# Performance work log

Hardware: AMD Instinct MI355X
Metric: run time of the kernel (lower is better)

## Reference

```python
import jax, jax.numpy as jnp
import numpy as np

B, I, O, G = 4096, 256, 256, 32


def setup_inputs() -> dict:
    key = jax.random.key(0)
    k1, k2, k3, k4 = jax.random.split(key, 4)
    x = jax.random.normal(k1, (B, I), dtype=jnp.float32)
    fouriercoeffs = jax.random.normal(k2, (2, O, I, G), dtype=jnp.float32) / (np.sqrt(I) * np.sqrt(G))
    bias = jnp.zeros((1, O), dtype=jnp.float32)
    mask = jnp.ones((I, O), dtype=jnp.float32)
    # scale_base = mu/sqrt(I) + sigma*(rand*2-1)/sqrt(I), mu=0, sigma=1
    scale_base = (jax.random.uniform(k3, (I, O), dtype=jnp.float32) * 2.0 - 1.0) / np.sqrt(I)
    scale_fft = jnp.ones((I, O), dtype=jnp.float32) * (1.0 / np.sqrt(I)) * mask
    return {"x": x, "fouriercoeffs": fouriercoeffs, "bias": bias, "mask": mask,
            "scale_base": scale_base, "scale_fft": scale_fft}


def reference(x, fouriercoeffs, bias, mask, scale_base, scale_fft):
    gridsize = fouriercoeffs.shape[-1]
    k = jnp.arange(1, gridsize + 1, dtype=x.dtype)          # (G,)
    kx = x[:, :, None] * k                                   # (B, I, G)
    c = jnp.cos(kx)
    s = jnp.sin(kx)
    # einsum 'dbik,djik->bij' with d=2 split into cos/sin parts
    y = jnp.einsum('bik,jik->bij', c, fouriercoeffs[0]) \
        + jnp.einsum('bik,jik->bij', s, fouriercoeffs[1])    # (B, I, O)
    base = jax.nn.silu(x)                                     # SiLU base branch
    y = scale_base[None, :, :] * base[:, :, None] + scale_fft[None, :, :] * y
    y = (mask[None, :, :] * y).sum(axis=1)                    # sum over inputdim -> (B, O)
    y = y + bias
    return y
```

## Files before the change

### kernel.cpp

```cpp
#include <hip/hip_runtime.h>
#include <stdint.h>


#define I_DIM 256
#define O_DIM 256
#define G_DIM 32
#define B_DIM 4096

#define BM 128
#define BN 128
#define KSPLIT 16
#define ICH 16
#define PITCH 72

typedef short s8v __attribute__((ext_vector_type(8)));
typedef float f4v __attribute__((ext_vector_type(4)));

__device__ __forceinline__ uint32_t pack2bf16(float a, float b) {
  uint32_t ua = __builtin_bit_cast(uint32_t, a);
  uint32_t ub = __builtin_bit_cast(uint32_t, b);
  ua += 0x7FFFu + ((ua >> 16) & 1u);
  ub += 0x7FFFu + ((ub >> 16) & 1u);
  return (ua >> 16) | (ub & 0xFFFF0000u);
}
__device__ __forceinline__ unsigned short bf16_rne(float a) {
  uint32_t ua = __builtin_bit_cast(uint32_t, a);
  ua += 0x7FFFu + ((ua >> 16) & 1u);
  return (unsigned short)(ua >> 16);
}
__device__ __forceinline__ uint32_t cvtpk_bf16(float a, float b) {
  uint32_t r;
  asm("v_cvt_pk_bf16_f32 %0, %1, %2" : "=v"(r) : "v"(a), "v"(b));
  return r;
}
__device__ __forceinline__ float silu_f(float v) { return v / (1.0f + __expf(-v)); }

__device__ __forceinline__ void gen_feat_store(float xv, uint4* Ar, int c0, int xr) {
  const int half = c0 >> 2;
  float s1, c1, s17, c17;
  __sincosf(xv, &s1, &c1);
  __sincosf(17.f * xv, &s17, &c17);
  const float m2 = 2.f * c1;
  float fA0 = half ? s1 : c1;
  float fA1 = m2 * fA0 - (half ? 0.f : 1.f);
  float fB0 = half ? s17 : c17;
  float fB1 = half ? (s17 * c1 + c17 * s1)
                   : (c17 * c1 - s17 * s1);
  #pragma unroll
  for (int q = 0; q < 2; ++q) {
    uint32_t wa0 = cvtpk_bf16(fA0, fA1);
    uint32_t wb0 = cvtpk_bf16(fB0, fB1);
    float tA2 = m2 * fA1 - fA0, tB2 = m2 * fB1 - fB0;
    float tA3 = m2 * tA2 - fA1, tB3 = m2 * tB2 - fB1;
    uint32_t wa1 = cvtpk_bf16(tA2, tA3);
    uint32_t wb1 = cvtpk_bf16(tB2, tB3);
    fA0 = m2 * tA3 - tA2;  fB0 = m2 * tB3 - tB2;
    fA1 = m2 * fA0 - tA3;  fB1 = m2 * fB0 - tB3;
    uint32_t wa2 = cvtpk_bf16(fA0, fA1);
    uint32_t wb2 = cvtpk_bf16(fB0, fB1);
    float uA2 = m2 * fA1 - fA0, uB2 = m2 * fB1 - fB0;
    float uA3 = m2 * uA2 - fA1, uB3 = m2 * uB2 - fB1;
    uint32_t wa3 = cvtpk_bf16(uA2, uA3);
    uint32_t wb3 = cvtpk_bf16(uB2, uB3);
    Ar[(c0 + q) ^ xr]     = make_uint4(wa0, wa1, wa2, wa3);
    Ar[(c0 + 2 + q) ^ xr] = make_uint4(wb0, wb1, wb2, wb3);
    fA0 = m2 * uA3 - uA2;  fB0 = m2 * uB3 - uB2;
    fA1 = m2 * fA0 - uA3;  fB1 = m2 * fB0 - uB3;
  }
}

__global__ __launch_bounds__(256) void prep_bs_kernel(
    const float* __restrict__ fc, const float* __restrict__ mask,
    const float* __restrict__ sfft, short* __restrict__ Bp)
{
  const int gid = blockIdx.x * 256 + threadIdx.x;
  const int e = gid & 3;
  const int p = gid >> 2;
  const int i = p >> 8, j = p & 255;
  const int d = e >> 1;
  const int koff = (e & 1) * 16;
  const size_t ij = (size_t)i * O_DIM + j;
  const float sf = sfft[ij] * mask[ij];
  const float* src = fc + ((size_t)d * (O_DIM * I_DIM)
                          + (size_t)j * I_DIM + i) * G_DIM + koff;
  uint32_t w[8];
  #pragma unroll
  for (int q = 0; q < 4; ++q) {
    float4 v = ((const float4*)src)[q];
    w[2*q]   = pack2bf16(v.x * sf, v.y * sf);
    w[2*q+1] = pack2bf16(v.z * sf, v.w * sf);
  }
  const int h = j >> 6, r = j & 63;
  const int cb = d * 4 + (e & 1) * 2;
  short* dst = Bp + ((size_t)i * 4 + h) * 4096;
  *(uint4*)&dst[(cb * 64 + r) * 8]       = make_uint4(w[0], w[1], w[2], w[3]);
  *(uint4*)&dst[((cb + 1) * 64 + r) * 8] = make_uint4(w[4], w[5], w[6], w[7]);
}

__global__ __launch_bounds__(256, 4) void kan_main8(
    const float* __restrict__ x,
    const short* __restrict__ Bp,
    const float* __restrict__ mask,
    const float* __restrict__ scale_base,
    unsigned short* __restrict__ partial)
{
  __shared__ short A_lds[2][BM * 64];

  const int tid = threadIdx.x;
  const int bx  = blockIdx.x;
  const int kc  = bx & 15;
  const int bn  = (bx >> 4) & 1;
  const int bm  = bx >> 5;
  const int i0  = kc * ICH;

  const int lane = tid & 63;
  const int wave = tid >> 6;
  const int wm   = wave & 1;
  const int wn   = wave >> 1;
  const int l15  = lane & 15;
  const int quad = lane >> 4;

  f4v acc[4][4];
  #pragma unroll
  for (int a = 0; a < 4; ++a)
    #pragma unroll
    for (int b = 0; b < 4; ++b)
      acc[a][b] = (f4v){0.f, 0.f, 0.f, 0.f};

  const int row  = tid >> 1;
  const int half = tid & 1;
  const int mg   = bm * BM + row;
  const int jg   = bn * BN + row;
  const int xr   = row & 7;

  const float* xrow = x + (size_t)mg * I_DIM + i0;
  const int c0 = half * 4;

  const short* bbase = Bp + ((size_t)i0 * 4 + (size_t)(bn * 2 + wn)) * 4096;

  gen_feat_store(xrow[0], (uint4*)&A_lds[0][row * 64], c0, xr);
  float xnxt = xrow[1];

  for (int it = 0; it < ICH; ++it) {
    __syncthreads();

    const short* bsl = bbase + (size_t)it * 16384;

    s8v b0[4];
    #pragma unroll
    for (int tn = 0; tn < 4; ++tn)
      b0[tn] = *(const s8v*)&bsl[(quad * 64 + tn * 16 + l15) * 8];

    if (it + 1 < ICH) {
      gen_feat_store(xnxt, (uint4*)&A_lds[(it + 1) & 1][row * 64], c0, xr);
      if (it + 2 < ICH) xnxt = xrow[it + 2];
    }

    const short* Ac = &A_lds[it & 1][0];
    __builtin_amdgcn_s_setprio(1);

    s8v b1[4];
    #pragma unroll
    for (int tn = 0; tn < 4; ++tn)
      b1[tn] = *(const s8v*)&bsl[((4 + quad) * 64 + tn * 16 + l15) * 8];

    {
      s8v a[4];
      #pragma unroll
      for (int tm = 0; tm < 4; ++tm) {
        const int r = wm * 64 + tm * 16 + l15;
        a[tm] = *(const s8v*)&Ac[r * 64 + ((quad ^ (r & 7)) * 8)];
      }
      #pragma unroll
      for (int tm = 0; tm < 4; ++tm)
        #pragma unroll
        for (int tn = 0; tn < 4; ++tn)
          acc[tm][tn] = __builtin_amdgcn_mfma_f32_16x16x32_bf16(a[tm], b0[tn], acc[tm][tn], 0, 0, 0);
    }
    {
      s8v a[4];
      #pragma unroll
      for (int tm = 0; tm < 4; ++tm) {
        const int r = wm * 64 + tm * 16 + l15;
        a[tm] = *(const s8v*)&Ac[r * 64 + (((4 + quad) ^ (r & 7)) * 8)];
      }
      #pragma unroll
      for (int tm = 0; tm < 4; ++tm)
        #pragma unroll
        for (int tn = 0; tn < 4; ++tn)
          acc[tm][tn] = __builtin_amdgcn_mfma_f32_16x16x32_bf16(a[tm], b1[tn], acc[tm][tn], 0, 0, 0);
    }
    __builtin_amdgcn_s_setprio(0);
  }

  __syncthreads();
  {
    const float* xb = xrow + half * 8;
    float4 v0 = ((const float4*)xb)[0];
    float4 v1 = ((const float4*)xb)[1];
    uint32_t a0 = pack2bf16(silu_f(v0.x), silu_f(v0.y));
    uint32_t a1 = pack2bf16(silu_f(v0.z), silu_f(v0.w));
    uint32_t a2 = pack2bf16(silu_f(v1.x), silu_f(v1.y));
    uint32_t a3 = pack2bf16(silu_f(v1.z), silu_f(v1.w));
    uint4* Arow = (uint4*)&A_lds[0][row * 64];
    Arow[half ^ xr]       = make_uint4(a0, a1, a2, a3);
    Arow[(2 + half) ^ xr] = make_uint4(0, 0, 0, 0);

    uint32_t w[4];
    #pragma unroll
    for (int p = 0; p < 4; ++p) {
      const int ia = i0 + half * 8 + 2 * p;
      const size_t o0 = (size_t)ia * O_DIM + jg;
      const size_t o1 = o0 + O_DIM;
      w[p] = pack2bf16(scale_base[o0] * mask[o0], scale_base[o1] * mask[o1]);
    }
    uint4* Brow = (uint4*)&A_lds[1][row * 64];
    Brow[half ^ xr]       = make_uint4(w[0], w[1], w[2], w[3]);
    Brow[(2 + half) ^ xr] = make_uint4(0, 0, 0, 0);
  }
  __syncthreads();
  {
    __builtin_amdgcn_s_setprio(1);
    s8v a[4], b[4];
    #pragma unroll
    for (int tm = 0; tm < 4; ++tm) {
      const int r = wm * 64 + tm * 16 + l15;
      a[tm] = *(const s8v*)&A_lds[0][r * 64 + ((quad ^ (r & 7)) * 8)];
    }
    #pragma unroll
    for (int tn = 0; tn < 4; ++tn) {
      const int r = wn * 64 + tn * 16 + l15;
      b[tn] = *(const s8v*)&A_lds[1][r * 64 + ((quad ^ (r & 7)) * 8)];
    }
    #pragma unroll
    for (int tm = 0; tm < 4; ++tm)
      #pragma unroll
      for (int tn = 0; tn < 4; ++tn)
        acc[tm][tn] = __builtin_amdgcn_mfma_f32_16x16x32_bf16(a[tm], b[tn], acc[tm][tn], 0, 0, 0);
    __builtin_amdgcn_s_setprio(0);
  }

  unsigned short* pbase = partial + (size_t)kc * B_DIM * O_DIM;
  #pragma unroll
  for (int tm = 0; tm < 4; ++tm) {
    #pragma unroll
    for (int tn = 0; tn < 4; ++tn) {
      const int n_g = bn * BN + wn * 64 + tn * 16 + l15;
      f4v v = acc[tm][tn];
      #pragma unroll
      for (int r = 0; r < 4; ++r) {
        const int m_g = bm * BM + wm * 64 + tm * 16 + quad * 4 + r;
        pbase[(size_t)m_g * O_DIM + n_g] = bf16_rne(v[r]);
      }
    }
  }
}

__global__ __launch_bounds__(256) void reduce_kernel(
    const unsigned short* __restrict__ partial, const float* __restrict__ bias,
    float* __restrict__ out)
{
  const int g  = blockIdx.x * 256 + threadIdx.x;
  const int m  = g >> 5;
  const int n8 = (g & 31) << 3;
  const unsigned short* p = partial + (size_t)m * O_DIM + n8;

  float acc[8];
  {
    float4 b0 = ((const float4*)(bias + n8))[0];
    float4 b1 = ((const float4*)(bias + n8))[1];
    acc[0] = b0.x; acc[1] = b0.y; acc[2] = b0.z; acc[3] = b0.w;
    acc[4] = b1.x; acc[5] = b1.y; acc[6] = b1.z; acc[7] = b1.w;
  }
  #pragma unroll
  for (int kc = 0; kc < KSPLIT; ++kc) {
    const uint4 v = *(const uint4*)(p + (size_t)kc * (B_DIM * O_DIM));
    acc[0] += __builtin_bit_cast(float, v.x << 16);
    acc[1] += __builtin_bit_cast(float, v.x & 0xFFFF0000u);
    acc[2] += __builtin_bit_cast(float, v.y << 16);
    acc[3] += __builtin_bit_cast(float, v.y & 0xFFFF0000u);
    acc[4] += __builtin_bit_cast(float, v.z << 16);
    acc[5] += __builtin_bit_cast(float, v.z & 0xFFFF0000u);
    acc[6] += __builtin_bit_cast(float, v.w << 16);
    acc[7] += __builtin_bit_cast(float, v.w & 0xFFFF0000u);
  }
  float* o = out + (size_t)m * O_DIM + n8;
  ((float4*)o)[0] = make_float4(acc[0], acc[1], acc[2], acc[3]);
  ((float4*)o)[1] = make_float4(acc[4], acc[5], acc[6], acc[7]);
}

__device__ __forceinline__ void gen_feat(float xv, int half, uint32_t* fb) {
  float s, c;
  __sincosf(xv, &s, &c);
  const float m2 = 2.f * c;
  float f0 = half ? s : c;
  float f1 = m2 * f0 - (half ? 0.f : 1.f);
  fb[0] = cvtpk_bf16(f0, f1);
  #pragma unroll
  for (int p = 1; p < 16; ++p) {
    float f2 = m2 * f1 - f0;
    float f3 = m2 * f2 - f1;
    fb[p] = cvtpk_bf16(f2, f3);
    f0 = f2; f1 = f3;
  }
}

__global__ __launch_bounds__(256, 4) void kan_fft_fallback(
    const float* __restrict__ x, const float* __restrict__ fc,
    const float* __restrict__ bias, const float* __restrict__ mask,
    const float* __restrict__ scale_base, const float* __restrict__ scale_fft,
    float* __restrict__ out)
{
  __shared__ short A_lds[BM * PITCH];
  __shared__ short B_lds[BN * PITCH];

  const int tid = threadIdx.x;
  const int bx  = blockIdx.x;
  const int kc  = bx & 15;
  const int bn  = (bx >> 4) & 1;
  const int bm  = bx >> 5;
  const int i0  = kc * ICH;

  const int lane = tid & 63;
  const int wave = tid >> 6;
  const int wm   = wave & 1;
  const int wn   = wave >> 1;
  const int l15  = lane & 15;
  const int kgrp = (lane >> 4) * 8;

  f4v acc[4][4];
  #pragma unroll
  for (int a = 0; a < 4; ++a)
    #pragma unroll
    for (int b = 0; b < 4; ++b)
      acc[a][b] = (f4v){0.f, 0.f, 0.f, 0.f};

  const int row  = tid >> 1;
  const int half = tid & 1;
  const int mg   = bm * BM + row;
  const int jg   = bn * BN + row;

  const float* xrow   = x + (size_t)mg * I_DIM + i0;
  const float* fcbase = fc + (size_t)half * (O_DIM * I_DIM * G_DIM)
                           + ((size_t)jg * I_DIM + i0) * G_DIM;
  uint32_t* Arow = (uint32_t*)&A_lds[row * PITCH + half * 32];
  uint32_t* Brow = (uint32_t*)&B_lds[row * PITCH + half * 32];

  for (int it = 0; it < ICH; ++it) {
    __syncthreads();
    {
      uint32_t fb[16];
      gen_feat(xrow[it], half, fb);
      ((uint4*)Arow)[0] = make_uint4(fb[0],  fb[1],  fb[2],  fb[3]);
      ((uint4*)Arow)[1] = make_uint4(fb[4],  fb[5],  fb[6],  fb[7]);
      ((uint4*)Arow)[2] = make_uint4(fb[8],  fb[9],  fb[10], fb[11]);
      ((uint4*)Arow)[3] = make_uint4(fb[12], fb[13], fb[14], fb[15]);
    }
    {
      const int i = i0 + it;
      const size_t ij = (size_t)i * O_DIM + jg;
      const float sf  = scale_fft[ij] * mask[ij];
      const float* src = fcbase + it * G_DIM;
      uint32_t wb[16];
      #pragma unroll
      for (int q = 0; q < 8; ++q) {
        float4 v = ((const float4*)src)[q];
        wb[2*q]   = pack2bf16(v.x * sf, v.y * sf);
        wb[2*q+1] = pack2bf16(v.z * sf, v.w * sf);
      }
      ((uint4*)Brow)[0] = make_uint4(wb[0],  wb[1],  wb[2],  wb[3]);
      ((uint4*)Brow)[1] = make_uint4(wb[4],  wb[5],  wb[6],  wb[7]);
      ((uint4*)Brow)[2] = make_uint4(wb[8],  wb[9],  wb[10], wb[11]);
      ((uint4*)Brow)[3] = make_uint4(wb[12], wb[13], wb[14], wb[15]);
    }
    __syncthreads();
    #pragma unroll
    for (int ks = 0; ks < 2; ++ks) {
      s8v a[4], b[4];
      #pragma unroll
      for (int tm = 0; tm < 4; ++tm)
        a[tm] = *(const s8v*)&A_lds[(wm * 64 + tm * 16 + l15) * PITCH + ks * 32 + kgrp];
      #pragma unroll
      for (int tn = 0; tn < 4; ++tn)
        b[tn] = *(const s8v*)&B_lds[(wn * 64 + tn * 16 + l15) * PITCH + ks * 32 + kgrp];
      #pragma unroll
      for (int tm = 0; tm < 4; ++tm)
        #pragma unroll
        for (int tn = 0; tn < 4; ++tn)
          acc[tm][tn] = __builtin_amdgcn_mfma_f32_16x16x32_bf16(a[tm], b[tn], acc[tm][tn], 0, 0, 0);
    }
  }

  __syncthreads();
  {
    const float* xb = xrow + half * 8;
    float4 v0 = ((const float4*)xb)[0];
    float4 v1 = ((const float4*)xb)[1];
    uint32_t a0 = pack2bf16(silu_f(v0.x), silu_f(v0.y));
    uint32_t a1 = pack2bf16(silu_f(v0.z), silu_f(v0.w));
    uint32_t a2 = pack2bf16(silu_f(v1.x), silu_f(v1.y));
    uint32_t a3 = pack2bf16(silu_f(v1.z), silu_f(v1.w));
    ((uint4*)&A_lds[row * PITCH + half * 8])[0]      = make_uint4(a0, a1, a2, a3);
    ((uint4*)&A_lds[row * PITCH + 16 + half * 8])[0] = make_uint4(0, 0, 0, 0);
    uint32_t w[4];
    #pragma unroll
    for (int p = 0; p < 4; ++p) {
      const int ia = i0 + half * 8 + 2 * p;
      const size_t o0 = (size_t)ia * O_DIM + jg;
      const size_t o1 = o0 + O_DIM;
      w[p] = pack2bf16(scale_base[o0] * mask[o0], scale_base[o1] * mask[o1]);
    }
    ((uint4*)&B_lds[row * PITCH + half * 8])[0]      = make_uint4(w[0], w[1], w[2], w[3]);
    ((uint4*)&B_lds[row * PITCH + 16 + half * 8])[0] = make_uint4(0, 0, 0, 0);
  }
  __syncthreads();
  {
    s8v a[4], b[4];
    #pragma unroll
    for (int tm = 0; tm < 4; ++tm)
      a[tm] = *(const s8v*)&A_lds[(wm * 64 + tm * 16 + l15) * PITCH + kgrp];
    #pragma unroll
    for (int tn = 0; tn < 4; ++tn)
      b[tn] = *(const s8v*)&B_lds[(wn * 64 + tn * 16 + l15) * PITCH + kgrp];
    #pragma unroll
    for (int tm = 0; tm < 4; ++tm)
      #pragma unroll
      for (int tn = 0; tn < 4; ++tn)
        acc[tm][tn] = __builtin_amdgcn_mfma_f32_16x16x32_bf16(a[tm], b[tn], acc[tm][tn], 0, 0, 0);
  }

  const int quad = lane >> 4;
  #pragma unroll
  for (int tm = 0; tm < 4; ++tm) {
    #pragma unroll
    for (int tn = 0; tn < 4; ++tn) {
      const int n_g = bn * BN + wn * 64 + tn * 16 + l15;
      f4v v = acc[tm][tn];
      #pragma unroll
      for (int r = 0; r < 4; ++r) {
        const int m_g = bm * BM + wm * 64 + tm * 16 + quad * 4 + r;
        float val = v[r];
        if (kc == 0) val += bias[n_g];
        atomicAdd(&out[(size_t)m_g * O_DIM + n_g], val);
      }
    }
  }
}

extern "C" void kernel_launch(void* const* d_in, const int* in_sizes, int n_in,
                              void* d_out, int out_size, void* d_ws, size_t ws_size,
                              hipStream_t stream) {
  const float* x          = (const float*)d_in[0];
  const float* fc         = (const float*)d_in[1];
  const float* bias       = (const float*)d_in[2];
  const float* mask       = (const float*)d_in[3];
  const float* scale_base = (const float*)d_in[4];
  const float* scale_fft  = (const float*)d_in[5];
  float* out = (float*)d_out;

  const size_t BP_B    = (size_t)I_DIM * O_DIM * 64 * 2;
  const size_t PARTH_B = (size_t)KSPLIT * B_DIM * O_DIM * 2;

  if (ws_size >= BP_B + PARTH_B) {
    short*          Bp      = (short*)d_ws;
    unsigned short* partial = (unsigned short*)((char*)d_ws + BP_B);
    prep_bs_kernel<<<dim3(1024), dim3(256), 0, stream>>>(fc, mask, scale_fft, Bp);
    kan_main8<<<dim3(1024), dim3(256), 0, stream>>>(x, Bp, mask, scale_base, partial);
    reduce_kernel<<<dim3(512), dim3(256), 0, stream>>>(partial, bias, out);
  } else {
    hipMemsetAsync(d_out, 0, (size_t)out_size * sizeof(float), stream);
    kan_fft_fallback<<<dim3(1024), dim3(256), 0, stream>>>(
        x, fc, bias, mask, scale_base, scale_fft, out);
  }
}
```

Baseline: 123.4 us.

## Widen main kernel tile to full output width with 512-thread blocks

Each block now covers all 256 output columns with 8 waves instead of 128 columns with 4 waves. The A-side Fourier features (sincos plus Chebyshev recurrence) for a batch tile are computed once and shared across the full width, where before two blocks recomputed them. Feature generation is split across 4 threads per row, one recurrence chain each, so each thread does less serial work. The base-branch epilogue is done in two halves with extra barriers, and the larger blocks may reduce occupancy and raise register pressure.

```diff
diff --git a/kernel.cpp b/kernel.cpp
--- a/kernel.cpp
+++ b/kernel.cpp
@@ -8,7 +8,7 @@
 #define B_DIM 4096
 
 #define BM 128
-#define BN 128
+#define BN 256
 #define KSPLIT 16
 #define ICH 16
 #define PITCH 72
@@ -35,37 +35,38 @@
 }
 __device__ __forceinline__ float silu_f(float v) { return v / (1.0f + __expf(-v)); }
 
-__device__ __forceinline__ void gen_feat_store(float xv, uint4* Ar, int c0, int xr) {
-  const int half = c0 >> 2;
-  float s1, c1, s17, c17;
+__device__ __forceinline__ void gen_feat_chain(float xv, int half, int chain,
+                                               uint4* Ar, int c0, int xr) {
+  float s1, c1;
   __sincosf(xv, &s1, &c1);
-  __sincosf(17.f * xv, &s17, &c17);
   const float m2 = 2.f * c1;
-  float fA0 = half ? s1 : c1;
-  float fA1 = m2 * fA0 - (half ? 0.f : 1.f);
-  float fB0 = half ? s17 : c17;
-  float fB1 = half ? (s17 * c1 + c17 * s1)
-                   : (c17 * c1 - s17 * s1);
+  float f0, f1;
+  if (chain == 0) {
+    f0 = half ? s1 : c1;
+    f1 = m2 * f0 - (half ? 0.f : 1.f);
+  } else {
+    float s17, c17;
+    __sincosf(17.f * xv, &s17, &c17);
+    f0 = half ? s17 : c17;
+    f1 = half ? (s17 * c1 + c17 * s1)
+              : (c17 * c1 - s17 * s1);
+  }
+  const int sb = c0 + 2 * chain;
   #pragma unroll
   for (int q = 0; q < 2; ++q) {
-    uint32_t wa0 = cvtpk_bf16(fA0, fA1);
-    uint32_t wb0 = cvtpk_bf16(fB0, fB1);
-    float tA2 = m2 * fA1 - fA0, tB2 = m2 * fB1 - fB0;
-    float tA3 = m2 * tA2 - fA1, tB3 = m2 * tB2 - fB1;
-    uint32_t wa1 = cvtpk_bf16(tA2, tA3);
-    uint32_t wb1 = cvtpk_bf16(tB2, tB3);
-    fA0 = m2 * tA3 - tA2;  fB0 = m2 * tB3 - tB2;
-    fA1 = m2 * fA0 - tA3;  fB1 = m2 * fB0 - tB3;
-    uint32_t wa2 = cvtpk_bf16(fA0, fA1);
-    uint32_t wb2 = cvtpk_bf16(fB0, fB1);
-    float uA2 = m2 * fA1 - fA0, uB2 = m2 * fB1 - fB0;
-    float uA3 = m2 * uA2 - fA1, uB3 = m2 * uB2 - fB1;
-    uint32_t wa3 = cvtpk_bf16(uA2, uA3);
-    uint32_t wb3 = cvtpk_bf16(uB2, uB3);
-    Ar[(c0 + q) ^ xr]     = make_uint4(wa0, wa1, wa2, wa3);
-    Ar[(c0 + 2 + q) ^ xr] = make_uint4(wb0, wb1, wb2, wb3);
-    fA0 = m2 * uA3 - uA2;  fB0 = m2 * uB3 - uB2;
-    fA1 = m2 * fA0 - uA3;  fB1 = m2 * fB0 - uB3;
+    uint32_t w0 = cvtpk_bf16(f0, f1);
+    float t2 = m2 * f1 - f0;
+    float t3 = m2 * t2 - f1;
+    uint32_t w1 = cvtpk_bf16(t2, t3);
+    f0 = m2 * t3 - t2;
+    f1 = m2 * f0 - t3;
+    uint32_t w2 = cvtpk_bf16(f0, f1);
+    float u2 = m2 * f1 - f0;
+    float u3 = m2 * u2 - f1;
+    uint32_t w3 = cvtpk_bf16(u2, u3);
+    Ar[(sb + q) ^ xr] = make_uint4(w0, w1, w2, w3);
+    f0 = m2 * u3 - u2;
+    f1 = m2 * f0 - u3;
   }
 }
 
@@ -97,7 +98,7 @@
   *(uint4*)&dst[((cb + 1) * 64 + r) * 8] = make_uint4(w[4], w[5], w[6], w[7]);
 }
 
-__global__ __launch_bounds__(256, 4) void kan_main8(
+__global__ __launch_bounds__(512, 4) void kan_main9(
     const float* __restrict__ x,
     const short* __restrict__ Bp,
     const float* __restrict__ mask,
@@ -109,8 +110,7 @@
   const int tid = threadIdx.x;
   const int bx  = blockIdx.x;
   const int kc  = bx & 15;
-  const int bn  = (bx >> 4) & 1;
-  const int bm  = bx >> 5;
+  const int bm  = bx >> 4;
   const int i0  = kc * ICH;
 
   const int lane = tid & 63;
@@ -127,18 +127,19 @@
     for (int b = 0; b < 4; ++b)
       acc[a][b] = (f4v){0.f, 0.f, 0.f, 0.f};
 
-  const int row  = tid >> 1;
-  const int half = tid & 1;
-  const int mg   = bm * BM + row;
-  const int jg   = bn * BN + row;
-  const int xr   = row & 7;
+  const int row   = tid >> 2;
+  const int q4    = tid & 3;
+  const int half  = q4 & 1;
+  const int chain = q4 >> 1;
+  const int mg    = bm * BM + row;
+  const int xr    = row & 7;
+  const int c0    = half * 4;
 
   const float* xrow = x + (size_t)mg * I_DIM + i0;
-  const int c0 = half * 4;
-
-  const short* bbase = Bp + ((size_t)i0 * 4 + (size_t)(bn * 2 + wn)) * 4096;
-
-  gen_feat_store(xrow[0], (uint4*)&A_lds[0][row * 64], c0, xr);
+
+  const short* bbase = Bp + ((size_t)i0 * 4 + (size_t)wn) * 4096;
+
+  gen_feat_chain(xrow[0], half, chain, (uint4*)&A_lds[0][row * 64], c0, xr);
   float xnxt = xrow[1];
 
   for (int it = 0; it < ICH; ++it) {
@@ -152,7 +153,7 @@
       b0[tn] = *(const s8v*)&bsl[(quad * 64 + tn * 16 + l15) * 8];
 
     if (it + 1 < ICH) {
-      gen_feat_store(xnxt, (uint4*)&A_lds[(it + 1) & 1][row * 64], c0, xr);
+      gen_feat_chain(xnxt, half, chain, (uint4*)&A_lds[(it + 1) & 1][row * 64], c0, xr);
       if (it + 2 < ICH) xnxt = xrow[it + 2];
     }
 
@@ -195,57 +196,66 @@
 
   __syncthreads();
   {
-    const float* xb = xrow + half * 8;
-    float4 v0 = ((const float4*)xb)[0];
-    float4 v1 = ((const float4*)xb)[1];
-    uint32_t a0 = pack2bf16(silu_f(v0.x), silu_f(v0.y));
-    uint32_t a1 = pack2bf16(silu_f(v0.z), silu_f(v0.w));
-    uint32_t a2 = pack2bf16(silu_f(v1.x), silu_f(v1.y));
-    uint32_t a3 = pack2bf16(silu_f(v1.z), silu_f(v1.w));
-    uint4* Arow = (uint4*)&A_lds[0][row * 64];
-    Arow[half ^ xr]       = make_uint4(a0, a1, a2, a3);
-    Arow[(2 + half) ^ xr] = make_uint4(0, 0, 0, 0);
-
-    uint32_t w[4];
-    #pragma unroll
-    for (int p = 0; p < 4; ++p) {
-      const int ia = i0 + half * 8 + 2 * p;
-      const size_t o0 = (size_t)ia * O_DIM + jg;
-      const size_t o1 = o0 + O_DIM;
-      w[p] = pack2bf16(scale_base[o0] * mask[o0], scale_base[o1] * mask[o1]);
-    }
-    uint4* Brow = (uint4*)&A_lds[1][row * 64];
-    Brow[half ^ xr]       = make_uint4(w[0], w[1], w[2], w[3]);
-    Brow[(2 + half) ^ xr] = make_uint4(0, 0, 0, 0);
-  }
-  __syncthreads();
-  {
-    __builtin_amdgcn_s_setprio(1);
-    s8v a[4], b[4];
-    #pragma unroll
-    for (int tm = 0; tm < 4; ++tm) {
-      const int r = wm * 64 + tm * 16 + l15;
-      a[tm] = *(const s8v*)&A_lds[0][r * 64 + ((quad ^ (r & 7)) * 8)];
-    }
+    uint4 val = make_uint4(0, 0, 0, 0);
+    if (q4 < 2) {
+      const float* xb = xrow + q4 * 8;
+      float4 v0 = ((const float4*)xb)[0];
+      float4 v1 = ((const float4*)xb)[1];
+      val = make_uint4(pack2bf16(silu_f(v0.x), silu_f(v0.y)),
+                       pack2bf16(silu_f(v0.z), silu_f(v0.w)),
+                       pack2bf16(silu_f(v1.x), silu_f(v1.y)),
+                       pack2bf16(silu_f(v1.z), silu_f(v1.w)));
+    }
+    ((uint4*)&A_lds[0][row * 64])[q4 ^ xr] = val;
+  }
+  #pragma unroll
+  for (int h2 = 0; h2 < 2; ++h2) {
+    {
+      const int jg = h2 * 128 + row;
+      uint4 val = make_uint4(0, 0, 0, 0);
+      if (q4 < 2) {
+        uint32_t w[4];
+        #pragma unroll
+        for (int p = 0; p < 4; ++p) {
+          const int ia = i0 + q4 * 8 + 2 * p;
+          const size_t o0 = (size_t)ia * O_DIM + jg;
+          const size_t o1 = o0 + O_DIM;
+          w[p] = pack2bf16(scale_base[o0] * mask[o0], scale_base[o1] * mask[o1]);
+        }
+        val = make_uint4(w[0], w[1], w[2], w[3]);
+      }
+      ((uint4*)&A_lds[1][row * 64])[q4 ^ xr] = val;
+    }
+    __syncthreads();
+    if ((wn >> 1) == h2) {
+      __builtin_amdgcn_s_setprio(1);
+      s8v a[4], b[4];
+      #pragma unroll
+      for (int tm = 0; tm < 4; ++tm) {
+        const int r = wm * 64 + tm * 16 + l15;
+        a[tm] = *(const s8v*)&A_lds[0][r * 64 + ((quad ^ (r & 7)) * 8)];
+      }
+      #pragma unroll
+      for (int tn = 0; tn < 4; ++tn) {
+        const int r = (wn & 1) * 64 + tn * 16 + l15;
+        b[tn] = *(const s8v*)&A_lds[1][r * 64 + ((quad ^ (r & 7)) * 8)];
+      }
+      #pragma unroll
+      for (int tm = 0; tm < 4; ++tm)
+        #pragma unroll
+        for (int tn = 0; tn < 4; ++tn)
+          acc[tm][tn] = __builtin_amdgcn_mfma_f32_16x16x32_bf16(a[tm], b[tn], acc[tm][tn], 0, 0, 0);
+      __builtin_amdgcn_s_setprio(0);
+    }
+    __syncthreads();
+  }
+
+  unsigned short* pbase = partial + (size_t)kc * B_DIM * O_DIM;
+  #pragma unroll
+  for (int tm = 0; tm < 4; ++tm) {
     #pragma unroll
     for (int tn = 0; tn < 4; ++tn) {
-      const int r = wn * 64 + tn * 16 + l15;
-      b[tn] = *(const s8v*)&A_lds[1][r * 64 + ((quad ^ (r & 7)) * 8)];
-    }
-    #pragma unroll
-    for (int tm = 0; tm < 4; ++tm)
-      #pragma unroll
-      for (int tn = 0; tn < 4; ++tn)
-        acc[tm][tn] = __builtin_amdgcn_mfma_f32_16x16x32_bf16(a[tm], b[tn], acc[tm][tn], 0, 0, 0);
-    __builtin_amdgcn_s_setprio(0);
-  }
-
-  unsigned short* pbase = partial + (size_t)kc * B_DIM * O_DIM;
-  #pragma unroll
-  for (int tm = 0; tm < 4; ++tm) {
-    #pragma unroll
-    for (int tn = 0; tn < 4; ++tn) {
-      const int n_g = bn * BN + wn * 64 + tn * 16 + l15;
+      const int n_g = wn * 64 + tn * 16 + l15;
       f4v v = acc[tm][tn];
       #pragma unroll
       for (int r = 0; r < 4; ++r) {
@@ -312,7 +322,7 @@
     float* __restrict__ out)
 {
   __shared__ short A_lds[BM * PITCH];
-  __shared__ short B_lds[BN * PITCH];
+  __shared__ short B_lds[BM * PITCH];
 
   const int tid = threadIdx.x;
   const int bx  = blockIdx.x;
@@ -338,7 +348,7 @@
   const int row  = tid >> 1;
   const int half = tid & 1;
   const int mg   = bm * BM + row;
-  const int jg   = bn * BN + row;
+  const int jg   = bn * 128 + row;
 
   const float* xrow   = x + (size_t)mg * I_DIM + i0;
   const float* fcbase = fc + (size_t)half * (O_DIM * I_DIM * G_DIM)
@@ -434,7 +444,7 @@
   for (int tm = 0; tm < 4; ++tm) {
     #pragma unroll
     for (int tn = 0; tn < 4; ++tn) {
-      const int n_g = bn * BN + wn * 64 + tn * 16 + l15;
+      const int n_g = bn * 128 + wn * 64 + tn * 16 + l15;
       f4v v = acc[tm][tn];
       #pragma unroll
       for (int r = 0; r < 4; ++r) {
@@ -465,7 +475,7 @@
     short*          Bp      = (short*)d_ws;
     unsigned short* partial = (unsigned short*)((char*)d_ws + BP_B);
     prep_bs_kernel<<<dim3(1024), dim3(256), 0, stream>>>(fc, mask, scale_fft, Bp);
-    kan_main8<<<dim3(1024), dim3(256), 0, stream>>>(x, Bp, mask, scale_base, partial);
+    kan_main9<<<dim3(512), dim3(512), 0, stream>>>(x, Bp, mask, scale_base, partial);
     reduce_kernel<<<dim3(512), dim3(256), 0, stream>>>(partial, bias, out);
   } else {
     hipMemsetAsync(d_out, 0, (size_t)out_size * sizeof(float), stream);
```

Result: no change. 121.5 us (median of 2 runs) (-1.5%).
